# Kernel optimization log

Measured on AMD Instinct MI355X. Metric: run time of the kernel, lower is better.

The kernel has to match this reference:

```python
import jax, jax.numpy as jnp
import numpy as np

B, T, D, TY = 64, 512, 96, 512
H, DK = 4, 32            # num_heads, embed_dim_per_head
E = H * DK               # embed_dim = 128
P = 2                    # function='L' -> 2 coefficients
L, HID = 64, 128         # latent_dim, hidden_dim


def setup_inputs() -> dict:
    key = jax.random.key(0)
    ks = jax.random.split(key, 16)
    inp = {
        "timesteps": jax.random.uniform(ks[0], (B, T), jnp.float32),
        "X": jax.random.normal(ks[1], (B, T, D), jnp.float32),
        "M": jax.random.randint(ks[2], (B, T, D), 0, 2).astype(jnp.float32),
        "y_time_steps": jax.random.uniform(ks[3], (B, TY), jnp.float32),
        # time_embedding: Linear(1, E)
        "te_w": jax.random.normal(ks[4], (E,), jnp.float32),
        "te_b": jax.random.normal(ks[5], (E,), jnp.float32) * 0.1,
        # learned query [1, P, E]
        "query": jax.random.normal(ks[6], (1, P, E), jnp.float32),
        # query_map / key_map: Linear(E, E), stored [in, out]
        "q_w": jax.random.normal(ks[7], (E, E), jnp.float32) / np.sqrt(E),
        "q_b": jax.random.normal(ks[8], (E,), jnp.float32) * 0.1,
        "k_w": jax.random.normal(ks[9], (E, E), jnp.float32) / np.sqrt(E),
        "k_b": jax.random.normal(ks[10], (E,), jnp.float32) * 0.1,
        # attn shared out: Linear(2D*H, L)
        "ow": jax.random.normal(ks[11], (2 * D * H, L), jnp.float32) / np.sqrt(2 * D * H),
        "ob": jnp.zeros((L,), jnp.float32),
        # decoder MLP: Linear(L,HID)+ReLU+Linear(HID,D)
        "w1": jax.random.normal(ks[12], (L, HID), jnp.float32) / np.sqrt(L),
        "b1": jnp.zeros((HID,), jnp.float32),
        "w2": jax.random.normal(ks[13], (HID, D), jnp.float32) / np.sqrt(HID),
        "b2": jnp.zeros((D,), jnp.float32),
    }
    return inp


def _fld_forward(timesteps, X, M, y_time_steps, te_w, te_b, query,
                 q_w, q_b, k_w, k_b, ow, ob, w1, b1, w2, b2):
    b, t, d = X.shape
    # time embedding: Linear(1,E), sin applied to indices i % H == 0
    emb = timesteps[..., None] * te_w + te_b               # [B,T,E]
    sin_idx = (jnp.arange(E) % H) == 0
    emb = jnp.where(sin_idx, jnp.sin(emb), emb)

    X_cat = jnp.concatenate([X, M], axis=-1)               # [B,T,2D]
    M_cat = jnp.concatenate([M, M], axis=-1)               # [B,T,2D]

    q = query @ q_w + q_b                                   # [1,P,E]
    k = emb @ k_w + k_b                                     # [B,T,E]
    q = q.reshape(1, P, H, DK).transpose(0, 2, 1, 3)        # [1,H,P,dk]
    k = k.reshape(b, t, H, DK).transpose(0, 2, 1, 3)        # [B,H,T,dk]

    scores = jnp.einsum('xhpd,bhtd->bhpt', q, k) / np.sqrt(DK)  # [B,H,P,T]
    # broadcast over value feature dim, mask per-feature, softmax over T
    logits = jnp.where(M_cat[:, None, None, :, :] == 0, -jnp.inf,
                       scores[..., None])                   # [B,H,P,T,2D]
    p = jax.nn.softmax(logits, axis=-2)
    xa = jnp.einsum('bhptf,btf->bhpf', p, X_cat)            # [B,H,P,2D]
    xa = xa.transpose(0, 2, 1, 3).reshape(b, P, H * 2 * d)  # [B,P,H*2D]
    coeffs = xa @ ow + ob                                   # [B,P,L]

    # function 'L': linear in y_time_steps
    x = coeffs[:, 0][:, None, :] + y_time_steps[:, :, None] * coeffs[:, 1][:, None, :]
    h1 = jax.nn.relu(x @ w1 + b1)
    return h1 @ w2 + b2                                     # [B,TY,D]


def reference(timesteps, X, M, y_time_steps, te_w, te_b, query,
              q_w, q_b, k_w, k_b, ow, ob, w1, b1, w2, b2):
    return _fld_forward(timesteps, X, M, y_time_steps, te_w, te_b, query,
                        q_w, q_b, k_w, k_b, ow, ob, w1, b1, w2, b2)
```

## Files before the change

kernel.cpp:

```cpp
#include <hip/hip_runtime.h>
#include <math.h>

#define B_   64
#define T_   512
#define D_   96
#define TY_  512
#define H_   4
#define DK_  32
#define E_   128
#define P_   2
#define L_   64
#define HID_ 128

#define WS_OB2P  1024
#define WS_PN    2048
#define WS_PD    395264

__global__ __launch_bounds__(256) void kphase1(
    const float* __restrict__ tsteps, const float* __restrict__ te_w,
    const float* __restrict__ te_b,   const float* __restrict__ X,
    const float* __restrict__ M,      const float* __restrict__ query,
    const float* __restrict__ q_w,    const float* __restrict__ q_b,
    const float* __restrict__ k_w,    const float* __restrict__ k_b,
    const float* __restrict__ ow,     float* __restrict__ ws)
{
    const int bi = blockIdx.x, tid = threadIdx.x;
    const int c = bi & 7, b = bi >> 3;

    __shared__ float qm[P_ * E_];
    __shared__ float w2q_s[E_ * 8];
    __shared__ float tw_s[E_], tb_s[E_], bq_s[8];
    __shared__ float w_s[8][64];
    __shared__ float red[96 * 17];
    __shared__ float obp2[4][64];

    {
        int p = tid >> 7, ep = tid & 127;
        float acc = q_b[ep];
        #pragma unroll 4
        for (int e = 0; e < E_; ++e)
            acc += query[p * E_ + e] * q_w[e * E_ + ep];
        qm[p * E_ + ep] = acc;
    }
    if (tid < E_) { tw_s[tid] = te_w[tid]; tb_s[tid] = te_b[tid]; }
    __syncthreads();
    const float rs = 0.17677669529663687f;
    #pragma unroll
    for (int i = 0; i < 4; ++i) {
        int idx = tid + i * 256;
        int e = idx >> 3, hp = idx & 7, h = hp >> 1, p = hp & 1;
        float acc = 0.f;
        #pragma unroll
        for (int dk = 0; dk < DK_; ++dk)
            acc += k_w[e * E_ + h * DK_ + dk] * qm[p * E_ + h * DK_ + dk];
        w2q_s[idx] = acc * rs;
    }
    if (tid < 8) {
        int hp = tid, h = hp >> 1, p = hp & 1;
        float acc = 0.f;
        #pragma unroll
        for (int dk = 0; dk < DK_; ++dk)
            acc += k_b[h * DK_ + dk] * qm[p * E_ + h * DK_ + dk];
        bq_s[hp] = acc * rs;
    }
    __syncthreads();

    {
        const int t = tid & 63, hpg = tid >> 6, hp0 = hpg * 2;
        const float tv = tsteps[b * T_ + c * 64 + t];
        float a0 = 0.f, a1 = 0.f;
        #pragma unroll 4
        for (int e = 0; e < E_; ++e) {
            float v = tv * tw_s[e] + tb_s[e];
            if ((e & 3) == 0) v = __sinf(v);
            float2 w = *(const float2*)&w2q_s[e * 8 + hp0];
            a0 += v * w.x;
            a1 += v * w.y;
        }
        w_s[hp0][t]     = __expf(a0 + bq_s[hp0]);
        w_s[hp0 + 1][t] = __expf(a1 + bq_s[hp0 + 1]);
    }
    __syncthreads();

    const int fid = tid & 127, slice = tid >> 7;
    float num[8] = {0.f, 0.f, 0.f, 0.f, 0.f, 0.f, 0.f, 0.f};
    float den[8] = {0.f, 0.f, 0.f, 0.f, 0.f, 0.f, 0.f, 0.f};
    if (fid < 96) {
        #pragma unroll 4
        for (int i = 0; i < 32; ++i) {
            int tl = slice + 2 * i;
            size_t base = ((size_t)(b * T_ + c * 64 + tl)) * D_ + fid;
            float m = M[base], x = X[base];
            float mx = m * x;
            #pragma unroll
            for (int hp = 0; hp < 8; ++hp) {
                num[hp] += w_s[hp][tl] * mx;
                den[hp] += w_s[hp][tl] * m;
            }
        }
    }
    __syncthreads();
    if (slice == 1 && fid < 96) {
        #pragma unroll
        for (int hp = 0; hp < 8; ++hp) {
            red[fid * 17 + hp]     = num[hp];
            red[fid * 17 + 8 + hp] = den[hp];
        }
    }
    __syncthreads();
    if (slice == 0 && fid < 96) {
        float* pN = ws + WS_PN + ((size_t)((b * 8 + c) * 8)) * 96;
        float* pD = ws + WS_PD + ((size_t)((b * 8 + c) * 8)) * 96;
        #pragma unroll
        for (int hp = 0; hp < 8; ++hp) {
            pN[hp * 96 + fid] = num[hp] + red[fid * 17 + hp];
            pD[hp * 96 + fid] = den[hp] + red[fid * 17 + 8 + hp];
        }
    }

    if (b == 0) {
        int sub = tid >> 6, l = tid & 63;
        float acc = 0.f;
        #pragma unroll
        for (int k = 0; k < 12; ++k) {
            int hj = c * 48 + sub * 12 + k;
            int h = hj / 96, j = hj - h * 96;
            acc += ow[(size_t)(h * 2 * D_ + D_ + j) * L_ + l];
        }
        obp2[sub][l] = acc;
        __syncthreads();
        if (sub == 0)
            ws[WS_OB2P + c * 64 + l] = obp2[0][l] + obp2[1][l]
                                     + obp2[2][l] + obp2[3][l];
    }
}

__global__ __launch_bounds__(256) void kphase2(
    const float* __restrict__ ow, const float* __restrict__ ob,
    const float* __restrict__ w1, const float* __restrict__ b1,
    const float* __restrict__ yts, const float* __restrict__ w2,
    const float* __restrict__ b2, const float* __restrict__ ws,
    float* __restrict__ out)
{
    __shared__ float w2_s[HID_ * D_];
    __shared__ float xa_s[8 * 96];
    __shared__ float cfp[4][2][64];
    __shared__ float cf_s[2][64];
    __shared__ float a0_s[HID_], a1_s[HID_];
    __shared__ float y_s[64];
    __shared__ float abp[2][2][128];

    const int bi = blockIdx.x, tid = threadIdx.x;
    const int b = bi >> 3;

    float4 wreg[12];
    {
        const float4* src = (const float4*)w2;
        #pragma unroll
        for (int i = 0; i < 12; ++i) wreg[i] = src[tid + i * 256];
    }
    if (tid < 64) y_s[tid] = yts[bi * 64 + tid];

    #pragma unroll
    for (int it = 0; it < 3; ++it) {
        int flat = tid + it * 256;
        int hp = flat / 96, f = flat - hp * 96;
        float n = 0.f, d = 0.f;
        #pragma unroll
        for (int cc = 0; cc < 8; ++cc) {
            n += ws[WS_PN + ((size_t)((b * 8 + cc) * 8 + hp)) * 96 + f];
            d += ws[WS_PD + ((size_t)((b * 8 + cc) * 8 + hp)) * 96 + f];
        }
        xa_s[flat] = n / d;
    }
    __syncthreads();

    #pragma unroll
    for (int it = 0; it < 2; ++it) {
        int idx = tid + it * 256;
        int h = idx >> 7, p = (idx >> 6) & 1, l = idx & 63;
        const float* xr = xa_s + (h * 2 + p) * 96;
        const float* owr = ow + (size_t)(h * 2 * D_) * L_ + l;
        float acc = 0.f;
        #pragma unroll 4
        for (int f = 0; f < 96; ++f)
            acc += xr[f] * owr[(size_t)f * L_];
        cfp[h][p][l] = acc;
    }
    __syncthreads();

    if (tid < 128) {
        int p = tid >> 6, l = tid & 63;
        float v = cfp[0][p][l] + cfp[1][p][l] + cfp[2][p][l]
                + cfp[3][p][l] + ob[l];
        #pragma unroll
        for (int g = 0; g < 8; ++g) v += ws[WS_OB2P + g * 64 + l];
        cf_s[p][l] = v;
    }
    __syncthreads();

    {
        int s = tid >> 7, j = tid & 127;
        float a0 = 0.f, a1 = 0.f;
        #pragma unroll 4
        for (int li = 0; li < 32; ++li) {
            int l = s * 32 + li;
            float wv = w1[l * HID_ + j];
            a0 += cf_s[0][l] * wv;
            a1 += cf_s[1][l] * wv;
        }
        abp[s][0][j] = a0;
        abp[s][1][j] = a1;
    }
    __syncthreads();

    if (tid < 128) {
        a0_s[tid] = abp[0][0][tid] + abp[1][0][tid] + b1[tid];
    } else {
        int j = tid - 128;
        a1_s[j] = abp[0][1][j] + abp[1][1][j];
    }
    {
        float4* dst = (float4*)w2_s;
        #pragma unroll
        for (int i = 0; i < 12; ++i) dst[tid + i * 256] = wreg[i];
    }
    __syncthreads();

    const int pos = tid & 63, ds = tid >> 6;
    const float y = y_s[pos];
    const float* wrow = w2_s + ds * 24;

    float acc[24];
    #pragma unroll
    for (int dd = 0; dd < 24; ++dd) acc[dd] = 0.f;

    #pragma unroll 4
    for (int j = 0; j < HID_; ++j) {
        float h = fmaxf(0.f, a0_s[j] + y * a1_s[j]);
        const float* wr = wrow + j * D_;
        #pragma unroll
        for (int q = 0; q < 6; ++q) {
            float4 w4 = *(const float4*)(wr + q * 4);
            acc[q * 4 + 0] += h * w4.x;
            acc[q * 4 + 1] += h * w4.y;
            acc[q * 4 + 2] += h * w4.z;
            acc[q * 4 + 3] += h * w4.w;
        }
    }

    float* op = out + ((size_t)(bi * 64 + pos)) * D_ + ds * 24;
    const float* bp = b2 + ds * 24;
    #pragma unroll
    for (int q = 0; q < 6; ++q) {
        float4 v;
        v.x = acc[q * 4 + 0] + bp[q * 4 + 0];
        v.y = acc[q * 4 + 1] + bp[q * 4 + 1];
        v.z = acc[q * 4 + 2] + bp[q * 4 + 2];
        v.w = acc[q * 4 + 3] + bp[q * 4 + 3];
        *(float4*)(op + q * 4) = v;
    }
}

extern "C" void kernel_launch(void* const* d_in, const int* in_sizes, int n_in,
                              void* d_out, int out_size, void* d_ws, size_t ws_size,
                              hipStream_t stream)
{
    const float* timesteps = (const float*)d_in[0];
    const float* X         = (const float*)d_in[1];
    const float* M         = (const float*)d_in[2];
    const float* yts       = (const float*)d_in[3];
    const float* te_w      = (const float*)d_in[4];
    const float* te_b      = (const float*)d_in[5];
    const float* query     = (const float*)d_in[6];
    const float* q_w       = (const float*)d_in[7];
    const float* q_b       = (const float*)d_in[8];
    const float* k_w       = (const float*)d_in[9];
    const float* k_b       = (const float*)d_in[10];
    const float* ow        = (const float*)d_in[11];
    const float* ob        = (const float*)d_in[12];
    const float* w1        = (const float*)d_in[13];
    const float* b1        = (const float*)d_in[14];
    const float* w2        = (const float*)d_in[15];
    const float* b2        = (const float*)d_in[16];
    float* out = (float*)d_out;
    float* ws  = (float*)d_ws;

    kphase1<<<512, 256, 0, stream>>>(timesteps, te_w, te_b, X, M, query,
                                     q_w, q_b, k_w, k_b, ow, ws);
    kphase2<<<512, 256, 0, stream>>>(ow, ob, w1, b1, yts, w2, b2, ws, out);
}
```

Before: 168.6 us.

## Replace decoder MLP with piecewise-linear table lookup over sorted ReLU breakpoints

Each hidden unit's pre-activation is linear in y, so the decoder output is piecewise linear in y with at most 128 breakpoints. A new per-batch kernel sorts the breakpoints and precomputes an intercept/slope table for each interval. A decode kernel then binary-searches y and does one fused multiply-add per output, removing the per-position 128x96 matmul. It also transposes the softmax weight buffer in shared memory so each step reads it with float4 loads, and it adds a third launch plus extra floating-point reassociation error from the prefix-sum table.

```diff
diff --git a/kernel.cpp b/kernel.cpp
--- a/kernel.cpp
+++ b/kernel.cpp
@@ -15,6 +15,9 @@
 #define WS_OB2P  1024
 #define WS_PN    2048
 #define WS_PD    395264
+#define WS_TAB   1048576
+#define RSZ_     25088
+#define TABOFF   256
 
 __global__ __launch_bounds__(256) void kphase1(
     const float* __restrict__ tsteps, const float* __restrict__ te_w,
@@ -30,7 +33,7 @@
     __shared__ float qm[P_ * E_];
     __shared__ float w2q_s[E_ * 8];
     __shared__ float tw_s[E_], tb_s[E_], bq_s[8];
-    __shared__ float w_s[8][64];
+    __shared__ float w_sB[64][8];
     __shared__ float red[96 * 17];
     __shared__ float obp2[4][64];
 
@@ -77,8 +80,9 @@
             a0 += v * w.x;
             a1 += v * w.y;
         }
-        w_s[hp0][t]     = __expf(a0 + bq_s[hp0]);
-        w_s[hp0 + 1][t] = __expf(a1 + bq_s[hp0 + 1]);
+        float e0 = __expf(a0 + bq_s[hp0]);
+        float e1 = __expf(a1 + bq_s[hp0 + 1]);
+        *(float2*)&w_sB[t][hp0] = make_float2(e0, e1);
     }
     __syncthreads();
 
@@ -92,10 +96,14 @@
             size_t base = ((size_t)(b * T_ + c * 64 + tl)) * D_ + fid;
             float m = M[base], x = X[base];
             float mx = m * x;
+            float4 wa = *(const float4*)&w_sB[tl][0];
+            float4 wb = *(const float4*)&w_sB[tl][4];
+            float wv[8];
+            *(float4*)&wv[0] = wa; *(float4*)&wv[4] = wb;
             #pragma unroll
             for (int hp = 0; hp < 8; ++hp) {
-                num[hp] += w_s[hp][tl] * mx;
-                den[hp] += w_s[hp][tl] * m;
+                num[hp] += wv[hp] * mx;
+                den[hp] += wv[hp] * m;
             }
         }
     }
@@ -135,31 +143,30 @@
     }
 }
 
-__global__ __launch_bounds__(256) void kphase2(
+__global__ __launch_bounds__(256) void kab(
     const float* __restrict__ ow, const float* __restrict__ ob,
     const float* __restrict__ w1, const float* __restrict__ b1,
-    const float* __restrict__ yts, const float* __restrict__ w2,
-    const float* __restrict__ b2, const float* __restrict__ ws,
-    float* __restrict__ out)
+    const float* __restrict__ w2, const float* __restrict__ b2,
+    float* __restrict__ ws)
 {
     __shared__ float w2_s[HID_ * D_];
     __shared__ float xa_s[8 * 96];
     __shared__ float cfp[4][2][64];
     __shared__ float cf_s[2][64];
-    __shared__ float a0_s[HID_], a1_s[HID_];
-    __shared__ float y_s[64];
     __shared__ float abp[2][2][128];
-
-    const int bi = blockIdx.x, tid = threadIdx.x;
-    const int b = bi >> 3;
-
-    float4 wreg[12];
+    __shared__ float ab0_s[HID_], ab1_s[HID_];
+    __shared__ float t_s[HID_], u_s[HID_], vt_s[HID_], c0_s[HID_];
+    __shared__ int   sidx_s[HID_];
+    __shared__ float base0_s[96], base1_s[96];
+
+    const int b = blockIdx.x, tid = threadIdx.x;
+
     {
         const float4* src = (const float4*)w2;
-        #pragma unroll
-        for (int i = 0; i < 12; ++i) wreg[i] = src[tid + i * 256];
-    }
-    if (tid < 64) y_s[tid] = yts[bi * 64 + tid];
+        float4* dst = (float4*)w2_s;
+        #pragma unroll
+        for (int i = 0; i < 12; ++i) dst[tid + i * 256] = src[tid + i * 256];
+    }
 
     #pragma unroll
     for (int it = 0; it < 3; ++it) {
@@ -215,49 +222,103 @@
     __syncthreads();
 
     if (tid < 128) {
-        a0_s[tid] = abp[0][0][tid] + abp[1][0][tid] + b1[tid];
+        ab0_s[tid] = abp[0][0][tid] + abp[1][0][tid] + b1[tid];
     } else {
         int j = tid - 128;
-        a1_s[j] = abp[0][1][j] + abp[1][1][j];
-    }
-    {
-        float4* dst = (float4*)w2_s;
-        #pragma unroll
-        for (int i = 0; i < 12; ++i) dst[tid + i * 256] = wreg[i];
-    }
-    __syncthreads();
-
-    const int pos = tid & 63, ds = tid >> 6;
-    const float y = y_s[pos];
-    const float* wrow = w2_s + ds * 24;
-
-    float acc[24];
-    #pragma unroll
-    for (int dd = 0; dd < 24; ++dd) acc[dd] = 0.f;
-
-    #pragma unroll 4
-    for (int j = 0; j < HID_; ++j) {
-        float h = fmaxf(0.f, a0_s[j] + y * a1_s[j]);
-        const float* wr = wrow + j * D_;
-        #pragma unroll
-        for (int q = 0; q < 6; ++q) {
-            float4 w4 = *(const float4*)(wr + q * 4);
-            acc[q * 4 + 0] += h * w4.x;
-            acc[q * 4 + 1] += h * w4.y;
-            acc[q * 4 + 2] += h * w4.z;
-            acc[q * 4 + 3] += h * w4.w;
-        }
-    }
-
-    float* op = out + ((size_t)(bi * 64 + pos)) * D_ + ds * 24;
-    const float* bp = b2 + ds * 24;
-    #pragma unroll
-    for (int q = 0; q < 6; ++q) {
+        ab1_s[j] = abp[0][1][j] + abp[1][1][j];
+    }
+    __syncthreads();
+
+    if (tid < 128) {
+        float a0 = ab0_s[tid], a1 = ab1_s[tid];
+        float t, u, vt, c0;
+        if (a1 > 0.f)      { t = -a0 / a1;  u =  a1; vt = -a0; c0 = 0.f; }
+        else if (a1 < 0.f) { t = -a0 / a1;  u = -a1; vt =  a0; c0 = 0.f; }
+        else               { t = INFINITY;  u = 0.f; vt = 0.f; c0 = fabsf(a0); }
+        t_s[tid] = t; u_s[tid] = u; vt_s[tid] = vt; c0_s[tid] = c0;
+    }
+    __syncthreads();
+
+    if (tid < 128) {
+        float tj = t_s[tid];
+        int r = 0;
+        for (int k = 0; k < 128; ++k) {
+            float tk = t_s[k];
+            r += (tk < tj) || (tk == tj && k < tid);
+        }
+        sidx_s[r] = tid;
+    }
+    __syncthreads();
+
+    float* reg = ws + WS_TAB + (size_t)b * RSZ_;
+    if (tid < 96) {
+        float g0 = 0.f, g1 = 0.f, ut = 0.f, vta = 0.f, cc2 = 0.f;
+        #pragma unroll 4
+        for (int j = 0; j < 128; ++j) {
+            float wv = w2_s[j * 96 + tid];
+            g0  += ab0_s[j] * wv;
+            g1  += ab1_s[j] * wv;
+            ut  += u_s[j]  * wv;
+            vta += vt_s[j] * wv;
+            cc2 += c0_s[j] * wv;
+        }
+        base0_s[tid] = 0.5f * (g0 + cc2 + vta) + b2[tid];
+        base1_s[tid] = 0.5f * (g1 - ut);
+    } else if (tid >= 128) {
+        int k = tid - 128;
+        reg[k] = t_s[sidx_s[k]];
+    }
+    __syncthreads();
+
+    if (tid < 96) {
+        float cur0 = base0_s[tid], cur1 = base1_s[tid];
+        float* tb = reg + TABOFF;
+        tb[tid] = cur0;
+        tb[96 + tid] = cur1;
+        #pragma unroll 4
+        for (int k = 0; k < 128; ++k) {
+            int j = sidx_s[k];
+            float wv = w2_s[j * 96 + tid];
+            cur0 -= vt_s[j] * wv;
+            cur1 += u_s[j] * wv;
+            tb[(k + 1) * 192 + tid]      = cur0;
+            tb[(k + 1) * 192 + 96 + tid] = cur1;
+        }
+    }
+}
+
+__global__ __launch_bounds__(256) void kdec(
+    const float* __restrict__ yts, const float* __restrict__ ws,
+    float* __restrict__ out)
+{
+    __shared__ float tS[128];
+    const int bi = blockIdx.x, tid = threadIdx.x;
+    const int b = bi >> 4;
+    const float* reg = ws + WS_TAB + (size_t)b * RSZ_;
+    if (tid < 128) tS[tid] = reg[tid];
+    __syncthreads();
+
+    const int pos = tid >> 3, d0 = (tid & 7) * 12;
+    const float y = yts[bi * 32 + pos];
+
+    int lo = 0, hi = 128;
+    #pragma unroll
+    for (int s = 0; s < 7; ++s) {
+        int mid = (lo + hi) >> 1;
+        if (tS[mid] < y) lo = mid + 1; else hi = mid;
+    }
+
+    const float* R = reg + TABOFF + lo * 192 + d0;
+    float* op = out + ((size_t)(bi * 32 + pos)) * D_ + d0;
+    #pragma unroll
+    for (int q = 0; q < 3; ++q) {
+        float4 r0 = *(const float4*)(R + q * 4);
+        float4 r1 = *(const float4*)(R + 96 + q * 4);
         float4 v;
-        v.x = acc[q * 4 + 0] + bp[q * 4 + 0];
-        v.y = acc[q * 4 + 1] + bp[q * 4 + 1];
-        v.z = acc[q * 4 + 2] + bp[q * 4 + 2];
-        v.w = acc[q * 4 + 3] + bp[q * 4 + 3];
+        v.x = r0.x + y * r1.x;
+        v.y = r0.y + y * r1.y;
+        v.z = r0.z + y * r1.z;
+        v.w = r0.w + y * r1.w;
         *(float4*)(op + q * 4) = v;
     }
 }
@@ -288,5 +349,6 @@
 
     kphase1<<<512, 256, 0, stream>>>(timesteps, te_w, te_b, X, M, query,
                                      q_w, q_b, k_w, k_b, ow, ws);
-    kphase2<<<512, 256, 0, stream>>>(ow, ob, w1, b1, yts, w2, b2, ws, out);
+    kab<<<B_, 256, 0, stream>>>(ow, ob, w1, b1, w2, b2, ws);
+    kdec<<<(B_ * TY_) / 32, 256, 0, stream>>>(yts, ws, out);
 }
```

Measured after the change: 165.6 us. No clear change (-1.8%).
